# Kernel optimization log

Measured on AMD Instinct MI355X. Metric: run time of the kernel, lower is better.

## Reference

```python
import jax, jax.numpy as jnp
import numpy as np

B, S, D_IN, D_OUT, H = 4, 2048, 1024, 1024, 16
D_HEAD = D_OUT // H


def setup_inputs() -> dict:
    key = jax.random.key(0)
    ks = jax.random.split(key, 6)
    sc = 0.02
    return {
        "x": jax.random.normal(ks[0], (B, S, D_IN), dtype=jnp.float32),
        "Wq": jax.random.normal(ks[1], (D_IN, D_OUT), dtype=jnp.float32) * sc,
        "Wk": jax.random.normal(ks[2], (D_IN, D_OUT), dtype=jnp.float32) * sc,
        "Wv": jax.random.normal(ks[3], (D_IN, D_OUT), dtype=jnp.float32) * sc,
        "Wo": jax.random.normal(ks[4], (D_OUT, D_OUT), dtype=jnp.float32) * sc,
        "bo": jnp.zeros((D_OUT,), dtype=jnp.float32),
    }


def reference(x, Wq, Wk, Wv, Wo, bo):
    n_batch, n_tok, _ = x.shape
    # QKV projections (no bias), reshape to [B, H, S, Dh]
    q = (x @ Wq).reshape(n_batch, n_tok, H, D_HEAD).transpose(0, 2, 1, 3)
    k = (x @ Wk).reshape(n_batch, n_tok, H, D_HEAD).transpose(0, 2, 1, 3)
    v = (x @ Wv).reshape(n_batch, n_tok, H, D_HEAD).transpose(0, 2, 1, 3)
    # scores [B, H, S, S], causal mask, scaled softmax
    scores = jnp.einsum('bhqd,bhkd->bhqk', q, k)
    causal = jnp.tril(jnp.ones((n_tok, n_tok), dtype=bool))
    scores = jnp.where(causal, scores, -jnp.inf)
    attn = jax.nn.softmax(scores / jnp.sqrt(jnp.float32(D_HEAD)), axis=-1)
    # dropout in eval mode -> identity
    ctx = jnp.einsum('bhqk,bhkd->bhqd', attn, v)
    ctx = ctx.transpose(0, 2, 1, 3).reshape(n_batch, n_tok, D_OUT)
    return ctx @ Wo + bo
```

## Files before the change

### kernel.cpp

```cpp
#include <hip/hip_runtime.h>


#define S_LEN 2048
#define NH 16
#define DH 64
#define DMODEL 1024
#define NB 4

typedef unsigned short u16;
typedef float f32x4 __attribute__((ext_vector_type(4)));
typedef short s16x8 __attribute__((ext_vector_type(8)));
typedef __bf16 bf16x8 __attribute__((ext_vector_type(8)));

__device__ __forceinline__ u16 f2bf(float f) {
  return __builtin_bit_cast(u16, (__bf16)f);
}

__device__ __forceinline__ f32x4 mfma16(s16x8 a, s16x8 b, f32x4 c) {
  return __builtin_amdgcn_mfma_f32_16x16x32_bf16(
      __builtin_bit_cast(bf16x8, a), __builtin_bit_cast(bf16x8, b), c, 0, 0, 0);
}

__device__ __forceinline__ void gload_lds16(void* lds, const void* g) {
  __builtin_amdgcn_global_load_lds(
      (const __attribute__((address_space(1))) void*)g,
      (__attribute__((address_space(3))) void*)lds, 16, 0, 0);
}

__device__ __forceinline__ s16x8 lds_frag(const u16* lds, int row, int colb) {
  int addr = (row << 7) + (colb ^ ((row & 7) << 4));
  return *(const s16x8*)((const char*)lds + addr);
}

template <int ROWS>
__device__ __forceinline__ void stage_tile_swz(u16* lds, const u16* gbase, int ldg, int tid) {
  constexpr int CH = (ROWS * 128) / (256 * 16);
  #pragma unroll
  for (int it = 0; it < CH; ++it) {
    int o = (tid + it * 256) * 16;
    int r = o >> 7;
    int c = o & 127;
    int csrc = c ^ ((r & 7) << 4);
    gload_lds16((char*)lds + o, (const char*)(gbase + (size_t)r * ldg) + csrc);
  }
}

__device__ __forceinline__ void gemm_core_128(const u16* A, const u16* Bt, int Kdim,
                                              int m0, int n0, u16* As, u16* Bs,
                                              f32x4 (&acc)[4][4], int tid) {
  const int lane = tid & 63;
  const int w = tid >> 6, wr = w >> 1, wc = w & 1;
  for (int k0 = 0; k0 < Kdim; k0 += 64) {
    __syncthreads();
    stage_tile_swz<128>(As, A + (size_t)m0 * Kdim + k0, Kdim, tid);
    stage_tile_swz<128>(Bs, Bt + (size_t)n0 * Kdim + k0, Kdim, tid);
    __syncthreads();
    #pragma unroll
    for (int ks = 0; ks < 2; ++ks) {
      s16x8 a[4], b[4];
      #pragma unroll
      for (int f = 0; f < 4; ++f) {
        a[f] = lds_frag(As, wr * 64 + f * 16 + (lane & 15), ks * 64 + ((lane >> 4) << 4));
        b[f] = lds_frag(Bs, wc * 64 + f * 16 + (lane & 15), ks * 64 + ((lane >> 4) << 4));
      }
      #pragma unroll
      for (int mf = 0; mf < 4; ++mf)
        #pragma unroll
        for (int nf = 0; nf < 4; ++nf)
          acc[mf][nf] = mfma16(a[mf], b[nf], acc[mf][nf]);
    }
  }
}

__global__ __launch_bounds__(256) void castx_kernel(const float4* __restrict__ x,
                                                    ushort4* __restrict__ xb) {
  int i = blockIdx.x * 256 + threadIdx.x;
  float4 v = x[i];
  ushort4 o;
  o.x = f2bf(v.x); o.y = f2bf(v.y); o.z = f2bf(v.z); o.w = f2bf(v.w);
  xb[i] = o;
}

__global__ __launch_bounds__(256) void wtrans_kernel(
    const float* __restrict__ W0, const float* __restrict__ W1,
    const float* __restrict__ W2, const float* __restrict__ W3,
    u16* __restrict__ T0, u16* __restrict__ T1, u16* __restrict__ T2, u16* __restrict__ T3) {
  int z = blockIdx.z;
  const float* W = (z == 0) ? W0 : (z == 1) ? W1 : (z == 2) ? W2 : W3;
  u16* T = (z == 0) ? T0 : (z == 1) ? T1 : (z == 2) ? T2 : T3;
  __shared__ float t[32][33];
  int n0 = blockIdx.x << 5, k0 = blockIdx.y << 5;
  int tx = threadIdx.x & 31, ty = threadIdx.x >> 5;
  #pragma unroll
  for (int j = 0; j < 4; ++j)
    t[ty + (j << 3)][tx] = W[(size_t)(k0 + ty + (j << 3)) * DMODEL + n0 + tx];
  __syncthreads();
  #pragma unroll
  for (int j = 0; j < 4; ++j)
    T[(size_t)(n0 + ty + (j << 3)) * DMODEL + k0 + tx] = f2bf(t[tx][ty + (j << 3)]);
}

__global__ __launch_bounds__(256) void proj_qkv_kernel(
    const u16* __restrict__ xb, const u16* __restrict__ WqT, const u16* __restrict__ WkT,
    const u16* __restrict__ WvT, u16* __restrict__ Qo, u16* __restrict__ Ko,
    u16* __restrict__ Vo) {
  __shared__ u16 As[128 * 64];
  __shared__ u16 Bs[128 * 64];
  int z = blockIdx.z;
  const u16* Bt = (z == 0) ? WqT : (z == 1) ? WkT : WvT;
  u16* out = (z == 0) ? Qo : (z == 1) ? Ko : Vo;
  float scale = (z == 0) ? 0.18033688f : 1.0f;
  int f = blockIdx.y * 8 + blockIdx.x;
  int wg = ((f & 7) << 6) + (f >> 3);
  int m0 = (wg >> 3) << 7, n0 = (wg & 7) << 7;
  int tid = threadIdx.x, lane = tid & 63, w = tid >> 6, wr = w >> 1, wc = w & 1;
  f32x4 acc[4][4] = {};
  gemm_core_128(xb, Bt, DMODEL, m0, n0, As, Bs, acc, tid);
  #pragma unroll
  for (int mf = 0; mf < 4; ++mf)
    #pragma unroll
    for (int nf = 0; nf < 4; ++nf)
      #pragma unroll
      for (int i = 0; i < 4; ++i) {
        int rm = m0 + wr * 64 + mf * 16 + ((lane >> 4) << 2) + i;
        int cn = n0 + wc * 64 + nf * 16 + (lane & 15);
        int bb = rm >> 11, s = rm & (S_LEN - 1);
        int h = cn >> 6, d = cn & 63;
        out[((size_t)((bb << 4) + h) << 17) + ((size_t)s << 6) + d] =
            f2bf(acc[mf][nf][i] * scale);
      }
}

__global__ __launch_bounds__(256) void vtrans_kernel(const u16* __restrict__ V,
                                                     u16* __restrict__ Vt) {
  __shared__ u16 t[64][72];
  int s0 = blockIdx.x << 6;
  size_t bh = blockIdx.y;
  const u16* Vb = V + (bh << 17);
  u16* Vtb = Vt + (bh << 17);
  int tid = threadIdx.x;
  #pragma unroll
  for (int it = 0; it < 2; ++it) {
    int o = (tid + (it << 8)) << 3;
    int r = o >> 6, c = o & 63;
    const ushort4* p = (const ushort4*)(Vb + (((size_t)(s0 + r)) << 6) + c);
    ushort4 v0 = p[0], v1 = p[1];
    t[r][c + 0] = v0.x; t[r][c + 1] = v0.y; t[r][c + 2] = v0.z; t[r][c + 3] = v0.w;
    t[r][c + 4] = v1.x; t[r][c + 5] = v1.y; t[r][c + 6] = v1.z; t[r][c + 7] = v1.w;
  }
  __syncthreads();
  #pragma unroll
  for (int it = 0; it < 2; ++it) {
    int o = (tid + (it << 8)) << 3;
    int d = o >> 6, sl = o & 63;
    ushort4 a, b;
    a.x = t[sl + 0][d]; a.y = t[sl + 1][d]; a.z = t[sl + 2][d]; a.w = t[sl + 3][d];
    b.x = t[sl + 4][d]; b.y = t[sl + 5][d]; b.z = t[sl + 6][d]; b.w = t[sl + 7][d];
    ushort4* q = (ushort4*)(Vtb + ((size_t)d << 11) + s0 + sl);
    q[0] = a; q[1] = b;
  }
}

__global__ __launch_bounds__(512, 4) void attn_kernel(const u16* __restrict__ Q,
                                                      const u16* __restrict__ K,
                                                      const u16* __restrict__ Vt,
                                                      u16* __restrict__ ctx) {
  __shared__ u16 Ks[2][64 * 64];
  __shared__ u16 Vts[2][64 * 64];
  __shared__ u16 Ps[8][16 * 64];
  int bh = blockIdx.x, pid = blockIdx.y;
  int tid = threadIdx.x, lane = tid & 63, w = tid >> 6;
  const u16* Qb = Q + ((size_t)bh << 17);
  const u16* Kb = K + ((size_t)bh << 17);
  const u16* Vtb = Vt + ((size_t)bh << 17);
  int bb = bh >> 4, h = bh & 15;
  u16* Pw = Ps[w];

  s16x8 onesf;
  #pragma unroll
  for (int j = 0; j < 8; ++j) onesf[j] = (short)0x3F80;

  auto stage = [&](int buf, int k0) {
    int o = tid << 4;
    int r = o >> 7, c = o & 127;
    int csrc = c ^ ((r & 7) << 4);
    gload_lds16((char*)Ks[buf] + o, (const char*)(Kb + ((size_t)(k0 + r) << 6)) + csrc);
    gload_lds16((char*)Vts[buf] + o, (const char*)(Vtb + ((size_t)r << 11) + k0) + csrc);
  };

  for (int ph = 0; ph < 2; ++ph) {
    int qblk = ph ? (15 - pid) : pid;
    int q0 = qblk << 7;
    int qw = q0 + (w << 4);

    s16x8 qf[2];
    #pragma unroll
    for (int ks = 0; ks < 2; ++ks) {
      int row = qw + (lane & 15);
      int col = ks * 32 + ((lane >> 4) << 3);
      qf[ks] = *(const s16x8*)(Qb + ((size_t)row << 6) + col);
    }

    f32x4 acc_o[4] = {};
    f32x4 acc_l = {};

    int ntiles = (q0 >> 6) + 2;
    int cur = 0;
    stage(0, 0);
    __syncthreads();
    for (int t = 0; t < ntiles; ++t) {
      int k0 = t << 6;
      if (t + 1 < ntiles) stage(cur ^ 1, (t + 1) << 6);

      bool active = (k0 <= qw + 15);
      if (active) {
        const u16* Kc = Ks[cur];
        const u16* Vc = Vts[cur];
        f32x4 sc[4] = {};
        #pragma unroll
        for (int ks = 0; ks < 2; ++ks) {
          s16x8 kf[4];
          #pragma unroll
          for (int nf = 0; nf < 4; ++nf)
            kf[nf] = lds_frag(Kc, nf * 16 + (lane & 15), ks * 64 + ((lane >> 4) << 4));
          __builtin_amdgcn_s_setprio(1);
          #pragma unroll
          for (int nf = 0; nf < 4; ++nf)
            sc[nf] = mfma16(qf[ks], kf[nf], sc[nf]);
          __builtin_amdgcn_s_setprio(0);
        }

        bool need_mask = (k0 + 63) > qw;
        if (need_mask) {
          #pragma unroll
          for (int i = 0; i < 4; ++i) {
            int q = qw + ((lane >> 4) << 2) + i;
            #pragma unroll
            for (int nf = 0; nf < 4; ++nf) {
              int kv = k0 + nf * 16 + (lane & 15);
              sc[nf][i] = (kv <= q) ? sc[nf][i] : -3.0e38f;
            }
          }
        }
        #pragma unroll
        for (int nf = 0; nf < 4; ++nf)
          #pragma unroll
          for (int i = 0; i < 4; ++i)
            sc[nf][i] = __builtin_amdgcn_exp2f(sc[nf][i]);

        #pragma unroll
        for (int nf = 0; nf < 4; ++nf)
          #pragma unroll
          for (int i = 0; i < 4; ++i) {
            int r = ((lane >> 4) << 2) + i;
            int cb = (nf * 16 + (lane & 15)) << 1;
            *(u16*)((char*)Pw + (r << 7) + (cb ^ ((r & 7) << 4))) = f2bf(sc[nf][i]);
          }
        asm volatile("s_waitcnt lgkmcnt(0)" ::: "memory");
        __builtin_amdgcn_sched_barrier(0);

        #pragma unroll
        for (int ks = 0; ks < 2; ++ks) {
          s16x8 pf = lds_frag(Pw, lane & 15, ks * 64 + ((lane >> 4) << 4));
          s16x8 vf[4];
          #pragma unroll
          for (int nf = 0; nf < 4; ++nf)
            vf[nf] = lds_frag(Vc, nf * 16 + (lane & 15), ks * 64 + ((lane >> 4) << 4));
          __builtin_amdgcn_s_setprio(1);
          #pragma unroll
          for (int nf = 0; nf < 4; ++nf)
            acc_o[nf] = mfma16(pf, vf[nf], acc_o[nf]);
          acc_l = mfma16(pf, onesf, acc_l);
          __builtin_amdgcn_s_setprio(0);
        }
      }
      __syncthreads();
      cur ^= 1;
    }

    #pragma unroll
    for (int i = 0; i < 4; ++i) acc_l[i] = 1.0f / acc_l[i];
    #pragma unroll
    for (int nf = 0; nf < 4; ++nf)
      #pragma unroll
      for (int i = 0; i < 4; ++i) {
        int q = qw + ((lane >> 4) << 2) + i;
        int d = nf * 16 + (lane & 15);
        float v = acc_o[nf][i] * acc_l[i];
        ctx[(((size_t)(bb << 11) + q) << 10) + (h << 6) + d] = f2bf(v);
      }
  }
}

__global__ __launch_bounds__(256) void proj_out_kernel(const u16* __restrict__ ctx,
                                                       const u16* __restrict__ WoT,
                                                       const float* __restrict__ bo,
                                                       float* __restrict__ out) {
  __shared__ u16 As[128 * 64];
  __shared__ u16 Bs[128 * 64];
  int f = blockIdx.y * 8 + blockIdx.x;
  int wg = ((f & 7) << 6) + (f >> 3);
  int m0 = (wg >> 3) << 7, n0 = (wg & 7) << 7;
  int tid = threadIdx.x, lane = tid & 63, w = tid >> 6, wr = w >> 1, wc = w & 1;
  f32x4 acc[4][4] = {};
  gemm_core_128(ctx, WoT, DMODEL, m0, n0, As, Bs, acc, tid);
  #pragma unroll
  for (int mf = 0; mf < 4; ++mf)
    #pragma unroll
    for (int nf = 0; nf < 4; ++nf)
      #pragma unroll
      for (int i = 0; i < 4; ++i) {
        int rm = m0 + wr * 64 + mf * 16 + ((lane >> 4) << 2) + i;
        int cn = n0 + wc * 64 + nf * 16 + (lane & 15);
        out[(size_t)rm * DMODEL + cn] = acc[mf][nf][i] + bo[cn];
      }
}

extern "C" void kernel_launch(void* const* d_in, const int* in_sizes, int n_in,
                              void* d_out, int out_size, void* d_ws, size_t ws_size,
                              hipStream_t stream) {
  const float* x  = (const float*)d_in[0];
  const float* Wq = (const float*)d_in[1];
  const float* Wk = (const float*)d_in[2];
  const float* Wv = (const float*)d_in[3];
  const float* Wo = (const float*)d_in[4];
  const float* bo = (const float*)d_in[5];
  float* out = (float*)d_out;

  char* ws = (char*)d_ws;
  const size_t SZ_T = (size_t)NB * S_LEN * DMODEL * 2;
  const size_t SZ_W = (size_t)DMODEL * DMODEL * 2;
  u16* xb  = (u16*)(ws);
  u16* WqT = (u16*)(ws + SZ_T);
  u16* WkT = (u16*)(ws + SZ_T + 1 * SZ_W);
  u16* WvT = (u16*)(ws + SZ_T + 2 * SZ_W);
  u16* WoT = (u16*)(ws + SZ_T + 3 * SZ_W);
  u16* Qb  = (u16*)(ws + 1 * SZ_T + 4 * SZ_W);
  u16* Kb  = (u16*)(ws + 2 * SZ_T + 4 * SZ_W);
  u16* Vb  = (u16*)(ws + 3 * SZ_T + 4 * SZ_W);
  u16* Vtb = (u16*)(ws + 4 * SZ_T + 4 * SZ_W);
  u16* ctx = xb;

  castx_kernel<<<dim3((NB * S_LEN * DMODEL / 4) / 256), dim3(256), 0, stream>>>(
      (const float4*)x, (ushort4*)xb);
  wtrans_kernel<<<dim3(32, 32, 4), dim3(256), 0, stream>>>(Wq, Wk, Wv, Wo,
                                                           WqT, WkT, WvT, WoT);
  proj_qkv_kernel<<<dim3(8, 64, 3), dim3(256), 0, stream>>>(xb, WqT, WkT, WvT,
                                                            Qb, Kb, Vb);
  vtrans_kernel<<<dim3(32, 64), dim3(256), 0, stream>>>(Vb, Vtb);
  attn_kernel<<<dim3(64, 8), dim3(512), 0, stream>>>(Qb, Kb, Vtb, ctx);
  proj_out_kernel<<<dim3(8, 64), dim3(256), 0, stream>>>(ctx, WoT, bo, out);
}
```

Baseline: 166.8 us.

## Pipeline projection GEMMs with triple-buffered LDS and a fused QKV launch

Replaces the synchronous 128x128 GEMM core with a 256x128-tile, 512-thread core. It triple-buffers A/B tiles in LDS, prefetching two k-steps ahead with direct global-to-LDS loads. Barriers are driven by explicit vmcnt waits, and wave priority is raised around the MFMA blocks. The three QKV projections become a single GEMM against the contiguous concatenated transposed weights, with the output routed per column. This aims to overlap memory loads with MFMA work and cut the load/compute serialisation of the old loop. The cost is roughly 144KB of LDS per block, so only one block fits per CU, and the out-projection grid shrinks to 256 blocks.

Result: faster. 160.0 us (-4.1%).

```diff
diff --git a/kernel.cpp b/kernel.cpp
--- a/kernel.cpp
+++ b/kernel.cpp
@@ -2,8 +2,6 @@
 
 
 #define S_LEN 2048
-#define NH 16
-#define DH 64
 #define DMODEL 1024
 #define NB 4
 
@@ -32,43 +30,76 @@
   return *(const s16x8*)((const char*)lds + addr);
 }
 
-template <int ROWS>
-__device__ __forceinline__ void stage_tile_swz(u16* lds, const u16* gbase, int ldg, int tid) {
-  constexpr int CH = (ROWS * 128) / (256 * 16);
-  #pragma unroll
-  for (int it = 0; it < CH; ++it) {
-    int o = (tid + it * 256) * 16;
-    int r = o >> 7;
-    int c = o & 127;
-    int csrc = c ^ ((r & 7) << 4);
-    gload_lds16((char*)lds + o, (const char*)(gbase + (size_t)r * ldg) + csrc);
-  }
-}
-
-__device__ __forceinline__ void gemm_core_128(const u16* A, const u16* Bt, int Kdim,
-                                              int m0, int n0, u16* As, u16* Bs,
-                                              f32x4 (&acc)[4][4], int tid) {
+struct G8 {
+  u16 As[3][256 * 64];
+  u16 Bs[3][128 * 64];
+};
+
+template <int NT>
+__device__ __forceinline__ void gemm8ph(const u16* __restrict__ A,
+                                        const u16* __restrict__ Bt,
+                                        int m0, int n0, G8& L,
+                                        f32x4 (&acc)[4][4], int tid) {
+  constexpr int K = NT * 64;
   const int lane = tid & 63;
-  const int w = tid >> 6, wr = w >> 1, wc = w & 1;
-  for (int k0 = 0; k0 < Kdim; k0 += 64) {
-    __syncthreads();
-    stage_tile_swz<128>(As, A + (size_t)m0 * Kdim + k0, Kdim, tid);
-    stage_tile_swz<128>(Bs, Bt + (size_t)n0 * Kdim + k0, Kdim, tid);
-    __syncthreads();
-    #pragma unroll
-    for (int ks = 0; ks < 2; ++ks) {
+  const int wr = (tid >> 6) >> 1, wc = (tid >> 6) & 1;
+
+  auto SA = [&](int buf, int kt) {
+    const u16* g = A + (size_t)m0 * K + kt * 64;
+    #pragma unroll
+    for (int it = 0; it < 4; ++it) {
+      int o = (tid + it * 512) << 4;
+      int r = o >> 7, c = o & 127;
+      gload_lds16((char*)L.As[buf] + o,
+                  (const char*)(g + (size_t)r * K) + (c ^ ((r & 7) << 4)));
+    }
+  };
+  auto SB = [&](int buf, int kt) {
+    const u16* g = Bt + (size_t)n0 * K + kt * 64;
+    #pragma unroll
+    for (int it = 0; it < 2; ++it) {
+      int o = (tid + it * 512) << 4;
+      int r = o >> 7, c = o & 127;
+      gload_lds16((char*)L.Bs[buf] + o,
+                  (const char*)(g + (size_t)r * K) + (c ^ ((r & 7) << 4)));
+    }
+  };
+
+  SA(0, 0); SB(0, 0);
+  SA(1, 1); SB(1, 1);
+  asm volatile("s_waitcnt vmcnt(6)" ::: "memory");
+  asm volatile("s_barrier" ::: "memory");
+
+  int cb = 0;
+  for (int t = 0; t < NT; ++t) {
+    const u16* Ac = L.As[cb];
+    const u16* Bc = L.Bs[cb];
+    int nxt = cb + 2; if (nxt >= 3) nxt -= 3;
+    bool pf = (t + 2 < NT);
+    #pragma unroll
+    for (int ph = 0; ph < 2; ++ph) {
       s16x8 a[4], b[4];
       #pragma unroll
       for (int f = 0; f < 4; ++f) {
-        a[f] = lds_frag(As, wr * 64 + f * 16 + (lane & 15), ks * 64 + ((lane >> 4) << 4));
-        b[f] = lds_frag(Bs, wc * 64 + f * 16 + (lane & 15), ks * 64 + ((lane >> 4) << 4));
-      }
+        a[f] = lds_frag(Ac, wr * 64 + f * 16 + (lane & 15), ph * 64 + ((lane >> 4) << 4));
+        b[f] = lds_frag(Bc, wc * 64 + f * 16 + (lane & 15), ph * 64 + ((lane >> 4) << 4));
+      }
+      if (pf) { if (ph == 0) SA(nxt, t + 2); else SB(nxt, t + 2); }
+      asm volatile("s_barrier" ::: "memory");
+      asm volatile("s_waitcnt lgkmcnt(0)" ::: "memory");
+      __builtin_amdgcn_sched_barrier(0);
+      __builtin_amdgcn_s_setprio(1);
       #pragma unroll
       for (int mf = 0; mf < 4; ++mf)
         #pragma unroll
         for (int nf = 0; nf < 4; ++nf)
           acc[mf][nf] = mfma16(a[mf], b[nf], acc[mf][nf]);
-    }
+      __builtin_amdgcn_s_setprio(0);
+    }
+    if (pf) asm volatile("s_waitcnt vmcnt(6)" ::: "memory");
+    else    asm volatile("s_waitcnt vmcnt(0)" ::: "memory");
+    asm volatile("s_barrier" ::: "memory");
+    cb = (cb + 1 == 3) ? 0 : cb + 1;
   }
 }
 
@@ -100,22 +131,17 @@
     T[(size_t)(n0 + ty + (j << 3)) * DMODEL + k0 + tx] = f2bf(t[tx][ty + (j << 3)]);
 }
 
-__global__ __launch_bounds__(256) void proj_qkv_kernel(
-    const u16* __restrict__ xb, const u16* __restrict__ WqT, const u16* __restrict__ WkT,
-    const u16* __restrict__ WvT, u16* __restrict__ Qo, u16* __restrict__ Ko,
-    u16* __restrict__ Vo) {
-  __shared__ u16 As[128 * 64];
-  __shared__ u16 Bs[128 * 64];
-  int z = blockIdx.z;
-  const u16* Bt = (z == 0) ? WqT : (z == 1) ? WkT : WvT;
-  u16* out = (z == 0) ? Qo : (z == 1) ? Ko : Vo;
-  float scale = (z == 0) ? 0.18033688f : 1.0f;
-  int f = blockIdx.y * 8 + blockIdx.x;
-  int wg = ((f & 7) << 6) + (f >> 3);
-  int m0 = (wg >> 3) << 7, n0 = (wg & 7) << 7;
-  int tid = threadIdx.x, lane = tid & 63, w = tid >> 6, wr = w >> 1, wc = w & 1;
+__global__ __launch_bounds__(512, 2) void qkv8_kernel(
+    const u16* __restrict__ xb, const u16* __restrict__ WqkvT,
+    u16* __restrict__ Qo, u16* __restrict__ Ko, u16* __restrict__ Vo) {
+  __shared__ G8 L;
+  int bid = blockIdx.x;
+  int f = (bid & 7) * 96 + (bid >> 3);
+  int m0 = (f / 24) << 8, n0 = (f % 24) << 7;
+  int tid = threadIdx.x, lane = tid & 63;
+  int wr = (tid >> 6) >> 1, wc = (tid >> 6) & 1;
   f32x4 acc[4][4] = {};
-  gemm_core_128(xb, Bt, DMODEL, m0, n0, As, Bs, acc, tid);
+  gemm8ph<16>(xb, WqkvT, m0, n0, L, acc, tid);
   #pragma unroll
   for (int mf = 0; mf < 4; ++mf)
     #pragma unroll
@@ -125,9 +151,11 @@
         int rm = m0 + wr * 64 + mf * 16 + ((lane >> 4) << 2) + i;
         int cn = n0 + wc * 64 + nf * 16 + (lane & 15);
         int bb = rm >> 11, s = rm & (S_LEN - 1);
-        int h = cn >> 6, d = cn & 63;
-        out[((size_t)((bb << 4) + h) << 17) + ((size_t)s << 6) + d] =
-            f2bf(acc[mf][nf][i] * scale);
+        int z = cn >> 10, c1 = cn & 1023;
+        int h = c1 >> 6, d = c1 & 63;
+        u16* out = (z == 0) ? Qo : (z == 1) ? Ko : Vo;
+        float v = acc[mf][nf][i] * ((z == 0) ? 0.18033688f : 1.0f);
+        out[((size_t)((bb << 4) + h) << 17) + ((size_t)s << 6) + d] = f2bf(v);
       }
 }
 
@@ -292,18 +320,18 @@
   }
 }
 
-__global__ __launch_bounds__(256) void proj_out_kernel(const u16* __restrict__ ctx,
-                                                       const u16* __restrict__ WoT,
-                                                       const float* __restrict__ bo,
-                                                       float* __restrict__ out) {
-  __shared__ u16 As[128 * 64];
-  __shared__ u16 Bs[128 * 64];
-  int f = blockIdx.y * 8 + blockIdx.x;
-  int wg = ((f & 7) << 6) + (f >> 3);
-  int m0 = (wg >> 3) << 7, n0 = (wg & 7) << 7;
-  int tid = threadIdx.x, lane = tid & 63, w = tid >> 6, wr = w >> 1, wc = w & 1;
+__global__ __launch_bounds__(512, 2) void out8_kernel(const u16* __restrict__ ctx,
+                                                      const u16* __restrict__ WoT,
+                                                      const float* __restrict__ bo,
+                                                      float* __restrict__ out) {
+  __shared__ G8 L;
+  int bid = blockIdx.x;
+  int f = (bid & 7) * 32 + (bid >> 3);
+  int m0 = (f >> 3) << 8, n0 = (f & 7) << 7;
+  int tid = threadIdx.x, lane = tid & 63;
+  int wr = (tid >> 6) >> 1, wc = (tid >> 6) & 1;
   f32x4 acc[4][4] = {};
-  gemm_core_128(ctx, WoT, DMODEL, m0, n0, As, Bs, acc, tid);
+  gemm8ph<16>(ctx, WoT, m0, n0, L, acc, tid);
   #pragma unroll
   for (int mf = 0; mf < 4; ++mf)
     #pragma unroll
@@ -345,9 +373,8 @@
       (const float4*)x, (ushort4*)xb);
   wtrans_kernel<<<dim3(32, 32, 4), dim3(256), 0, stream>>>(Wq, Wk, Wv, Wo,
                                                            WqT, WkT, WvT, WoT);
-  proj_qkv_kernel<<<dim3(8, 64, 3), dim3(256), 0, stream>>>(xb, WqT, WkT, WvT,
-                                                            Qb, Kb, Vb);
+  qkv8_kernel<<<dim3(768), dim3(512), 0, stream>>>(xb, WqT, Qb, Kb, Vb);
   vtrans_kernel<<<dim3(32, 64), dim3(256), 0, stream>>>(Vb, Vtb);
   attn_kernel<<<dim3(64, 8), dim3(512), 0, stream>>>(Qb, Kb, Vtb, ctx);
-  proj_out_kernel<<<dim3(8, 64), dim3(256), 0, stream>>>(ctx, WoT, bo, out);
-}
+  out8_kernel<<<dim3(256), dim3(512), 0, stream>>>(ctx, WoT, bo, out);
+}
```
